# Performance work log

Measured on AMD Instinct MI355X. Metric: run time of the kernel, lower is better.

The kernel has to match this reference:

```python
import jax, jax.numpy as jnp
import numpy as np

B, T = 32, 64
I, O, H = 64, 64, 512
N, W = 128, 64           # memory slots, slot width
IF = 3 * W + 6           # interface size


def setup_inputs() -> dict:
    key = jax.random.key(0)
    ks = jax.random.split(key, 6)
    s = 0.05
    return {
        "x": jax.random.normal(ks[0], (B, T, I), jnp.float32),
        "W_ih": jax.random.normal(ks[1], (4 * H, I + W), jnp.float32) * s,
        "W_hh": jax.random.normal(ks[2], (4 * H, H), jnp.float32) * s,
        "b_ih": jnp.zeros((4 * H,), jnp.float32),
        "b_hh": jnp.zeros((4 * H,), jnp.float32),
        "W_if": jax.random.normal(ks[3], (IF, H), jnp.float32) * s,
        "b_if": jnp.zeros((IF,), jnp.float32),
        "W_out": jax.random.normal(ks[4], (O, H + W), jnp.float32) * s,
        "b_out": jnp.zeros((O,), jnp.float32),
    }


def reference(x, W_ih, W_hh, b_ih, b_hh, W_if, b_if, W_out, b_out):
    Bb, Tt, _ = x.shape
    dt = x.dtype
    eye = jnp.eye(N, dtype=dt)
    batch_idx = jnp.arange(Bb)[:, None]

    def step(carry, x_t):
        h, c, mem, usage, prec, link, rw, rvec = carry
        # --- LSTM controller (PyTorch gate order i,f,g,o) ---
        inp = jnp.concatenate([x_t, rvec], axis=-1)
        gates = inp @ W_ih.T + h @ W_hh.T + b_ih + b_hh
        i_g, f_g, g_g, o_g = jnp.split(gates, 4, axis=-1)
        c = jax.nn.sigmoid(f_g) * c + jax.nn.sigmoid(i_g) * jnp.tanh(g_g)
        h = jax.nn.sigmoid(o_g) * jnp.tanh(c)
        itf = h @ W_if.T + b_if
        # --- parse interface ---
        erase = jax.nn.sigmoid(itf[:, :W])
        wvec = itf[:, W:2 * W]
        wg = jax.nn.sigmoid(itf[:, 2 * W])
        ag = jax.nn.sigmoid(itf[:, 2 * W + 1])
        rstr = jnp.log1p(jnp.exp(itf[:, 3 * W + 2]))  # softplus
        # --- allocation weighting (sort usage asc, shifted cumprod, scatter) ---
        idx = jnp.argsort(usage, axis=-1)
        usage_sorted = jnp.take_along_axis(usage, idx, axis=-1)
        cprod = jnp.cumprod(usage_sorted, axis=-1)
        cprod = jnp.concatenate([jnp.ones((Bb, 1), dt), cprod[:, :-1]], axis=-1)
        alloc_in_order = (1.0 - usage_sorted) * cprod
        alloc = jnp.zeros_like(usage).at[batch_idx, idx].set(alloc_in_order)
        ww = wg[:, None] * ag[:, None] * alloc  # [B,N]
        # --- erase + add write ---
        mem = mem * (1.0 - ww[:, :, None] * erase[:, None, :]) + ww[:, :, None] * wvec[:, None, :]
        usage = usage + (1.0 - usage) * ww
        # --- temporal link / precedence ---
        ww_ij = ww[:, :, None] + ww[:, None, :]
        link = (1.0 - ww_ij) * link + prec[:, :, None] * ww[:, None, :]
        link = link * (1.0 - eye)
        prec = (1.0 - ww.sum(-1, keepdims=True)) * prec + ww
        # --- read weights (NOTE: source uses itf[:, :W] as read key) ---
        rmode = jax.nn.softmax(itf[:, -3:], axis=-1)
        rkey = itf[:, :W]
        dot = jnp.einsum('bw,bnw->bn', rkey, mem)
        kn = jnp.linalg.norm(rkey, axis=-1, keepdims=True) + 1e-8
        mn = jnp.linalg.norm(mem, axis=-1) + 1e-8
        cw = jax.nn.softmax(dot / (kn * mn) * rstr[:, None], axis=-1)
        bw = jnp.einsum('bnm,bn->bm', link, rw)   # link^T @ rw
        fw = jnp.einsum('bnm,bm->bn', link, rw)   # link @ rw
        wts = rmode[:, 0:1] * bw + rmode[:, 1:2] * fw + rmode[:, 2:3] * cw + 1e-8
        wts = wts / wts.sum(-1, keepdims=True)
        rvec = jnp.einsum('bn,bnw->bw', wts, mem)
        out = jnp.concatenate([h, rvec], axis=-1) @ W_out.T + b_out
        return (h, c, mem, usage, prec, link, wts, rvec), out

    z = lambda *s: jnp.zeros(s, dt)
    carry0 = (z(Bb, H), z(Bb, H), z(Bb, N, W), z(Bb, N), z(Bb, N), z(Bb, N, N), z(Bb, N), z(Bb, W))
    _, outs = jax.lax.scan(step, carry0, jnp.swapaxes(x, 0, 1))
    return jnp.swapaxes(outs, 0, 1)  # [B,T,O]
```

## Files before the change

### kernel.cpp

```cpp
#include <hip/hip_runtime.h>
#include <math.h>

#define Bb 32
#define Tt 64
#define Ii 64
#define Oo 64
#define Hh 512
#define Nn 128
#define Wd 64
#define IFs 198
#define KV 640
#define G4 2048

#define NP1 128
#define NWG 160
#define NT 512
#define VST2 648

#define P2_MEM    0
#define P2_H      8320
#define P2_SCR    8896
#define P2_ITF    10944
#define P2_ERASE  11168
#define P2_WVEC   11232
#define P2_USAGE  11296
#define P2_PREC   11424
#define P2_RW     11552
#define P2_WW     11680
#define P2_SCAN   11808
#define P2_SS     11936
#define P2_SCAL   12064
#define P2_BIF    12080
#define P2_ALLOC  12304
#define P1_WIF    0
#define P1_BS     13464
#define P1_V      13720
#define P1_CC     15016
#define P1_HSL    15144
#define P1_PACC   15272
#define SMEM_FLOATS 17352
#define SMEM_BYTES (SMEM_FLOATS * 4)

#define S_WWSUM 0

__device__ __align__(16) float g_WT[KV * G4];
__device__ __align__(16) float g_bsum[G4];
typedef unsigned long long u64;
__device__ u64 g_h64[2 * Bb * Hh];
__device__ u64 g_rv64[Bb * Wd];
__device__ u64 g_if64[Bb * 8 * 200];

__device__ __forceinline__ float sigf(float v) { return 1.f / (1.f + expf(-v)); }

__device__ __forceinline__ u64 ldrelax(const u64* p) {
  return __hip_atomic_load(p, __ATOMIC_RELAXED, __HIP_MEMORY_SCOPE_AGENT);
}
__device__ __forceinline__ void tstore(u64* p, unsigned tag, float v) {
  u64 val = ((u64)tag << 32) | (u64)__float_as_uint(v);
  __hip_atomic_store(p, val, __ATOMIC_RELAXED, __HIP_MEMORY_SCOPE_AGENT);
}
__device__ __forceinline__ float fixwait(const u64* p, u64 v, unsigned tag) {
  while ((unsigned)(v >> 32) != tag) {
    __builtin_amdgcn_s_sleep(1);
    v = ldrelax(p);
  }
  return __uint_as_float((unsigned)(v & 0xffffffffu));
}

#define TIN 512
__global__ __launch_bounds__(TIN) void dnc_init(const float* __restrict__ W_ih,
                                                const float* __restrict__ W_hh,
                                                const float* __restrict__ b_ih,
                                                const float* __restrict__ b_hh) {
  __shared__ float tile[64][65];
  const int tid = threadIdx.x;
  int i0 = blockIdx.x * blockDim.x + tid;
  int st = gridDim.x * blockDim.x;
  for (int idx = i0; idx < G4; idx += st) g_bsum[idx] = b_ih[idx] + b_hh[idx];
  for (int idx = i0; idx < 2 * Bb * Hh; idx += st) g_h64[idx] = 0ull;
  for (int idx = i0; idx < Bb * Wd; idx += st) g_rv64[idx] = 0ull;
  for (int idx = i0; idx < Bb * 8 * 200; idx += st) g_if64[idx] = 0ull;

  for (int tileId = blockIdx.x; tileId < 320; tileId += gridDim.x) {
    int tc = tileId >> 5, tj = tileId & 31;
    for (int k = tid; k < 64 * 64; k += TIN) {
      int r = k >> 6, cl = k & 63;
      int j = tj * 64 + r, c = tc * 64 + cl;
      tile[r][cl] = (c < 128) ? W_ih[j * 128 + c] : W_hh[j * 512 + (c - 128)];
    }
    __syncthreads();
    for (int k = tid; k < 64 * 64; k += TIN) {
      int cl = k >> 6, rjj = k & 63;
      int c = tc * 64 + cl;
      int rp;
      if (c < 64) rp = (c >> 4) * 160 + 128 + (c & 15);
      else if (c < 128) { int cc = c - 64; rp = (cc >> 4) * 160 + 144 + (cc & 15); }
      else { int u = c - 128; rp = (u >> 7) * 160 + (u & 127); }
      g_WT[(size_t)rp * G4 + tj * 64 + rjj] = tile[rjj][cl];
    }
    __syncthreads();
  }
}

__global__ __launch_bounds__(NT) void dnc_main(const float* __restrict__ x,
                                               const float* __restrict__ W_if,
                                               const float* __restrict__ b_if,
                                               const float* __restrict__ W_out,
                                               const float* __restrict__ b_out,
                                               float* __restrict__ out) {
  extern __shared__ float sm[];
  const int tid = threadIdx.x;
  const int wg = blockIdx.x;

  if (wg < NP1) {
    const int jb = wg & 7;
    const int bb = wg >> 3;
    const int b0 = bb * 2;
    for (int i = tid; i < IFs * 64; i += NT) {
      int o = i >> 6, c = i & 63;
      sm[P1_WIF + o * 68 + c] = W_if[(size_t)o * Hh + jb * 64 + c];
    }
    if (tid < 64) {
      int gq = tid >> 4, m = tid & 15;
      ((float4*)(sm + P1_BS))[tid] = ((const float4*)g_bsum)[gq * 128 + jb * 16 + m];
    }
    if (tid < 128) sm[P1_CC + tid] = 0.f;
    __syncthreads();

    for (int t = 0; t < Tt; ++t) {
      {
        const u64* hsrc = g_h64 + (size_t)((t + 1) & 1) * (Bb * Hh);
        const int u = tid;
        const u64* a0 = hsrc + (size_t)b0 * Hh + u;
        const u64* a1 = hsrc + (size_t)(b0 + 1) * Hh + u;
        u64 v0 = ldrelax(a0), v1 = ldrelax(a1);
        float h0 = fixwait(a0, v0, (unsigned)t);
        float h1 = fixwait(a1, v1, (unsigned)t);
        const int rp = (u >> 7) * 160 + (u & 127);
        sm[P1_V + rp] = h0;
        sm[P1_V + VST2 + rp] = h1;
        if (tid < 128) {
          const int bl2 = tid >> 6, i = tid & 63;
          float xv = x[((size_t)(b0 + bl2) * Tt + t) * Ii + i];
          sm[P1_V + bl2 * VST2 + (i >> 4) * 160 + 128 + (i & 15)] = xv;
        }
      }
      __syncthreads();

      {
        const int fc = tid & 63, bl = (tid >> 6) & 1, ks = tid >> 7;
        const int lane = tid & 63;
        const int fcol = (fc >> 4) * 128 + jb * 16 + (fc & 15);
        const float* va = sm + P1_V + bl * VST2 + ks * 160;
        const float4* wp = (const float4*)g_WT + (size_t)(ks * 160) * (G4 / 4) + fcol;
        float4 a = {0.f, 0.f, 0.f, 0.f};
#pragma unroll 8
        for (int r = 0; r < 144; ++r) {
          float4 w4 = wp[(size_t)r * (G4 / 4)];
          float fv = va[r];
          a.x += w4.x * fv; a.y += w4.y * fv; a.z += w4.z * fv; a.w += w4.w * fv;
        }
        if (lane < 16) {
          const u64* rp = g_rv64 + (size_t)(b0 + bl) * Wd + ks * 16 + lane;
          float rv = fixwait(rp, ldrelax(rp), (unsigned)t);
          sm[P1_V + bl * VST2 + ks * 160 + 144 + lane] = rv;
        }
#pragma unroll
        for (int r = 144; r < 160; ++r) {
          float4 w4 = wp[(size_t)r * (G4 / 4)];
          float fv = va[r];
          a.x += w4.x * fv; a.y += w4.y * fv; a.z += w4.z * fv; a.w += w4.w * fv;
        }
        ((float4*)(sm + P1_PACC))[(ks * 2 + bl) * 65 + fc] = a;
      }
      __syncthreads();
      if (tid < 128) {
        const int bl = tid >> 6, l = tid & 63;
        const float* pb = sm + P1_PACC + bl * 260 + l;
        float gv0 = 0.f, gv1 = 0.f, gv2 = 0.f, gv3 = 0.f;
#pragma unroll
        for (int ks = 0; ks < 4; ++ks) {
          const float* pk = pb + ks * 520;
          gv0 += pk[0];
          gv1 += pk[64];
          gv2 += pk[128];
          gv3 += pk[192];
        }
        float ig = gv0 + sm[P1_BS + l];
        float fg = gv1 + sm[P1_BS + 64 + l];
        float gg = gv2 + sm[P1_BS + 128 + l];
        float og = gv3 + sm[P1_BS + 192 + l];
        float co = sm[P1_CC + bl * 64 + l];
        float cn = sigf(fg) * co + sigf(ig) * tanhf(gg);
        float hn = sigf(og) * tanhf(cn);
        sm[P1_CC + bl * 64 + l] = cn;
        sm[P1_HSL + bl * 64 + l] = hn;
        tstore(g_h64 + (size_t)(t & 1) * (Bb * Hh) + (size_t)(b0 + bl) * Hh + jb * 64 + l,
               (unsigned)(t + 1), hn);
      }
      __syncthreads();
      if (tid < 2 * IFs) {
        const int o = tid >> 1, bl = tid & 1;
        const float4* wr = (const float4*)(sm + P1_WIF + o * 68);
        const float4* h4 = (const float4*)(sm + P1_HSL + bl * 64);
        float acc = 0.f;
#pragma unroll 8
        for (int c4 = 0; c4 < 16; ++c4) {
          float4 w = wr[c4]; float4 h = h4[c4];
          acc += w.x * h.x + w.y * h.y + w.z * h.z + w.w * h.w;
        }
        tstore(g_if64 + ((size_t)(b0 + bl) * 8 + jb) * 200 + o, (unsigned)(t + 1), acc);
      }
    }
  } else {
    const int b = wg - NP1;
    float* SCR = sm + P2_SCR;
    float regL[32], regLT[32];
#pragma unroll
    for (int k = 0; k < 32; ++k) { regL[k] = 0.f; regLT[k] = 0.f; }
    for (int i = tid; i < Nn * 65; i += NT) sm[P2_MEM + i] = 0.f;
    if (tid < 128) { sm[P2_USAGE + tid] = 0.f; sm[P2_PREC + tid] = 0.f; sm[P2_RW + tid] = 0.f; }
    if (tid < IFs) sm[P2_BIF + tid] = b_if[tid];
    __syncthreads();
    if (tid < 64) {
      const int li = tid, i0 = 2 * li, i1 = i0 + 1;
      float u0 = sm[P2_USAGE + i0], u1 = sm[P2_USAGE + i1];
      int r0 = 0, r1 = 0;
      for (int jc = 0; jc < 32; ++jc) {
        float4 uj4 = *(const float4*)(sm + P2_USAGE + jc * 4);
#pragma unroll
        for (int e = 0; e < 4; ++e) {
          float uj = (&uj4.x)[e];
          int j = jc * 4 + e;
          r0 += (uj < u0 || (uj == u0 && j < i0)) ? 1 : 0;
          r1 += (uj < u1 || (uj == u1 && j < i1)) ? 1 : 0;
        }
      }
      sm[P2_SS + r0] = u0;
      sm[P2_SS + r1] = u1;
      float s0 = sm[P2_SS + i0], s1 = sm[P2_SS + i1];
      float p = s0 * s1;
#pragma unroll
      for (int off = 1; off < 64; off <<= 1) {
        float v = __shfl_up(p, off, 64);
        if (li >= off) p *= v;
      }
      float E = __shfl_up(p, 1, 64);
      if (li == 0) E = 1.f;
      sm[P2_SCAN + i0] = E * s0;
      sm[P2_SCAN + i1] = E * s0 * s1;
      float ex0 = (r0 > 0) ? sm[P2_SCAN + r0 - 1] : 1.f;
      float ex1 = (r1 > 0) ? sm[P2_SCAN + r1 - 1] : 1.f;
      sm[P2_ALLOC + i0] = (1.f - u0) * ex0;
      sm[P2_ALLOC + i1] = (1.f - u1) * ex1;
    }
    __syncthreads();

    for (int t = 0; t < Tt; ++t) {
      if (tid < 2 * IFs) {
        const int o = tid >> 1, hf = tid & 1;
        const u64* src = g_if64 + ((size_t)b * 8 + hf * 4) * 200 + o;
        u64 a0 = ldrelax(src), a1 = ldrelax(src + 200),
            a2 = ldrelax(src + 400), a3 = ldrelax(src + 600);
        float s = fixwait(src, a0, (unsigned)(t + 1))
                + fixwait(src + 200, a1, (unsigned)(t + 1))
                + fixwait(src + 400, a2, (unsigned)(t + 1))
                + fixwait(src + 600, a3, (unsigned)(t + 1));
        s += __shfl_xor(s, 1, 64);
        if (hf == 0) sm[P2_ITF + o] = s + sm[P2_BIF + o];
      }
      __syncthreads();
      float kn_r = 0.f, rstr_r = 0.f, rm0_r = 0.f, rm1_r = 0.f, rm2_r = 0.f;
      if (tid < 64) {
        const int li = tid, i0 = 2 * li, i1 = i0 + 1;
        float wgag = sigf(sm[P2_ITF + 128]) * sigf(sm[P2_ITF + 129]);
        float rs = sm[P2_ITF + 194];
        rstr_r = (rs > 20.f) ? rs : log1pf(expf(rs));
        float m0 = sm[P2_ITF + 195], m1 = sm[P2_ITF + 196], m2 = sm[P2_ITF + 197];
        float mx = fmaxf(m0, fmaxf(m1, m2));
        float e0 = expf(m0 - mx), e1 = expf(m1 - mx), e2 = expf(m2 - mx);
        float es = e0 + e1 + e2;
        rm0_r = e0 / es; rm1_r = e1 / es; rm2_r = e2 / es;
        float rk = sm[P2_ITF + li];
        sm[P2_ERASE + li] = sigf(rk);
        sm[P2_WVEC + li] = sm[P2_ITF + 64 + li];
        float sq = rk * rk;
#pragma unroll
        for (int off = 32; off > 0; off >>= 1) sq += __shfl_xor(sq, off, 64);
        kn_r = sqrtf(sq) + 1e-8f;
        float u0 = sm[P2_USAGE + i0], u1 = sm[P2_USAGE + i1];
        float w0 = wgag * sm[P2_ALLOC + i0];
        float w1 = wgag * sm[P2_ALLOC + i1];
        sm[P2_WW + i0] = w0; sm[P2_WW + i1] = w1;
        sm[P2_USAGE + i0] = u0 + (1.f - u0) * w0;
        sm[P2_USAGE + i1] = u1 + (1.f - u1) * w1;
        float wws = w0 + w1;
#pragma unroll
        for (int off = 32; off > 0; off >>= 1) wws += __shfl_xor(wws, off, 64);
        if (li == 0) sm[P2_SCAL + S_WWSUM] = wws;
      }
      __syncthreads();
      {
        const int n = tid & 127, ws = tid >> 7;
        float4 er[4], wv[4], kf[4];
#pragma unroll
        for (int r = 0; r < 4; ++r) {
          er[r] = *(const float4*)(sm + P2_ERASE + ws * 16 + r * 4);
          wv[r] = *(const float4*)(sm + P2_WVEC + ws * 16 + r * 4);
          kf[r] = *(const float4*)(sm + P2_ITF + ws * 16 + r * 4);
        }
        float wwn = sm[P2_WW + n];
        float dotp = 0.f, mnp = 0.f;
        const int base = P2_MEM + n * 65 + ws * 16;
#pragma unroll
        for (int q = 0; q < 16; ++q) {
          float m = sm[base + q];
          float ee = (&er[q >> 2].x)[q & 3];
          float vv = (&wv[q >> 2].x)[q & 3];
          float kk = (&kf[q >> 2].x)[q & 3];
          m = m * (1.f - wwn * ee) + wwn * vv;
          sm[base + q] = m;
          dotp += kk * m;
          mnp += m * m;
        }
        SCR[ws * 128 + n] = dotp;
        SCR[512 + ws * 128 + n] = mnp;
        const int m = n, ns = ws;
        float wwm = wwn;
        float prn = sm[P2_PREC + m];
        float bwp = 0.f, fwp = 0.f;
#pragma unroll
        for (int kq = 0; kq < 8; ++kq) {
          float4 ww4 = *(const float4*)(sm + P2_WW + ns * 32 + kq * 4);
          float4 pr4 = *(const float4*)(sm + P2_PREC + ns * 32 + kq * 4);
          float4 rw4 = *(const float4*)(sm + P2_RW + ns * 32 + kq * 4);
#pragma unroll
          for (int e = 0; e < 4; ++e) {
            int k = kq * 4 + e;
            int nn = ns * 32 + k;
            float wwo = (&ww4.x)[e];
            float pro = (&pr4.x)[e];
            float rwo = (&rw4.x)[e];
            float L = regL[k];
            L = (1.f - wwo - wwm) * L + pro * wwm;
            if (nn == m) L = 0.f;
            regL[k] = L;
            bwp += L * rwo;
            float LT = regLT[k];
            LT = (1.f - wwm - wwo) * LT + prn * wwo;
            if (nn == m) LT = 0.f;
            regLT[k] = LT;
            fwp += LT * rwo;
          }
        }
        SCR[1024 + ns * 128 + m] = bwp;
        SCR[1536 + ns * 128 + m] = fwp;
      }
      __syncthreads();
      if (tid < 64) {
        int i0 = 2 * tid, i1 = i0 + 1;
        float d0 = SCR[i0] + SCR[128 + i0] + SCR[256 + i0] + SCR[384 + i0];
        float d1 = SCR[i1] + SCR[128 + i1] + SCR[256 + i1] + SCR[384 + i1];
        float mn0 = sqrtf(SCR[512 + i0] + SCR[640 + i0] + SCR[768 + i0] + SCR[896 + i0]) + 1e-8f;
        float mn1 = sqrtf(SCR[512 + i1] + SCR[640 + i1] + SCR[768 + i1] + SCR[896 + i1]) + 1e-8f;
        float bw0 = SCR[1024 + i0] + SCR[1152 + i0] + SCR[1280 + i0] + SCR[1408 + i0];
        float bw1 = SCR[1024 + i1] + SCR[1152 + i1] + SCR[1280 + i1] + SCR[1408 + i1];
        float fw0 = SCR[1536 + i0] + SCR[1664 + i0] + SCR[1792 + i0] + SCR[1920 + i0];
        float fw1 = SCR[1536 + i1] + SCR[1664 + i1] + SCR[1792 + i1] + SCR[1920 + i1];
        float q0 = d0 / (kn_r * mn0) * rstr_r;
        float q1 = d1 / (kn_r * mn1) * rstr_r;
        float mx = fmaxf(q0, q1);
#pragma unroll
        for (int off = 32; off > 0; off >>= 1) mx = fmaxf(mx, __shfl_xor(mx, off, 64));
        float e0 = expf(q0 - mx), e1 = expf(q1 - mx);
        float es = e0 + e1;
#pragma unroll
        for (int off = 32; off > 0; off >>= 1) es += __shfl_xor(es, off, 64);
        float wv0 = rm0_r * bw0 + rm1_r * fw0 + rm2_r * (e0 / es) + 1e-8f;
        float wv1 = rm0_r * bw1 + rm1_r * fw1 + rm2_r * (e1 / es) + 1e-8f;
        float wsum = wv0 + wv1;
#pragma unroll
        for (int off = 32; off > 0; off >>= 1) wsum += __shfl_xor(wsum, off, 64);
        sm[P2_RW + i0] = wv0 / wsum;
        sm[P2_RW + i1] = wv1 / wsum;
      }
      __syncthreads();
      {
        const int w = tid & 63, ns8 = tid >> 6;
        float4 rw4[4];
#pragma unroll
        for (int r = 0; r < 4; ++r)
          rw4[r] = *(const float4*)(sm + P2_RW + ns8 * 16 + r * 4);
        float p = 0.f;
#pragma unroll
        for (int k = 0; k < 16; ++k)
          p += (&rw4[k >> 2].x)[k & 3] * sm[P2_MEM + (ns8 * 16 + k) * 65 + w];
        SCR[ns8 * 64 + w] = p;
      }
      __syncthreads();
      if (tid < 64) {
        float r = 0.f;
#pragma unroll
        for (int s2 = 0; s2 < 8; ++s2) r += SCR[s2 * 64 + tid];
        sm[P2_H + 512 + tid] = r;
        tstore(g_rv64 + (size_t)b * Wd + tid, (unsigned)(t + 1), r);
      } else if (tid < 320) {
        const int idx = tid - 64;
        const u64* hsrc = g_h64 + (size_t)(t & 1) * (Bb * Hh) + (size_t)b * Hh;
        const u64* a0 = hsrc + idx * 2;
        const u64* a1 = hsrc + idx * 2 + 1;
        u64 v0 = ldrelax(a0), v1 = ldrelax(a1);
        sm[P2_H + idx * 2] = fixwait(a0, v0, (unsigned)(t + 1));
        sm[P2_H + idx * 2 + 1] = fixwait(a1, v1, (unsigned)(t + 1));
      } else if (tid < 384) {
        const int li = tid - 320, i0 = 2 * li, i1 = i0 + 1;
        float u0 = sm[P2_USAGE + i0], u1 = sm[P2_USAGE + i1];
        int r0 = 0, r1 = 0;
        for (int jc = 0; jc < 32; ++jc) {
          float4 uj4 = *(const float4*)(sm + P2_USAGE + jc * 4);
#pragma unroll
          for (int e = 0; e < 4; ++e) {
            float uj = (&uj4.x)[e];
            int j = jc * 4 + e;
            r0 += (uj < u0 || (uj == u0 && j < i0)) ? 1 : 0;
            r1 += (uj < u1 || (uj == u1 && j < i1)) ? 1 : 0;
          }
        }
        sm[P2_SS + r0] = u0;
        sm[P2_SS + r1] = u1;
        float s0 = sm[P2_SS + i0], s1 = sm[P2_SS + i1];
        float p = s0 * s1;
#pragma unroll
        for (int off = 1; off < 64; off <<= 1) {
          float v = __shfl_up(p, off, 64);
          if (li >= off) p *= v;
        }
        float E = __shfl_up(p, 1, 64);
        if (li == 0) E = 1.f;
        sm[P2_SCAN + i0] = E * s0;
        sm[P2_SCAN + i1] = E * s0 * s1;
        float ex0 = (r0 > 0) ? sm[P2_SCAN + r0 - 1] : 1.f;
        float ex1 = (r1 > 0) ? sm[P2_SCAN + r1 - 1] : 1.f;
        sm[P2_ALLOC + i0] = (1.f - u0) * ex0;
        sm[P2_ALLOC + i1] = (1.f - u1) * ex1;
      } else {
        const int n = tid - 384;
        float wws = sm[P2_SCAL + S_WWSUM];
        sm[P2_PREC + n] = (1.f - wws) * sm[P2_PREC + n] + sm[P2_WW + n];
      }
      __syncthreads();
      {
        const int o = tid >> 3, seg = tid & 7;
        const float4* wrow = (const float4*)(W_out + (size_t)o * 576) + seg * 18;
        const float4* hb = (const float4*)(sm + P2_H) + seg * 18;
        float p = 0.f;
#pragma unroll
        for (int q = 0; q < 18; ++q) {
          float4 w = wrow[q]; float4 h = hb[q];
          p += w.x * h.x + w.y * h.y + w.z * h.z + w.w * h.w;
        }
        p += __shfl_down(p, 4, 8);
        p += __shfl_down(p, 2, 8);
        p += __shfl_down(p, 1, 8);
        if (seg == 0) out[((size_t)b * Tt + t) * Oo + o] = p + b_out[o];
      }
    }
  }
}

extern "C" void kernel_launch(void* const* d_in, const int* in_sizes, int n_in,
                              void* d_out, int out_size, void* d_ws, size_t ws_size,
                              hipStream_t stream) {
  (void)in_sizes; (void)n_in; (void)d_ws; (void)ws_size; (void)out_size;
  const float* x    = (const float*)d_in[0];
  const float* W_ih = (const float*)d_in[1];
  const float* W_hh = (const float*)d_in[2];
  const float* b_ih = (const float*)d_in[3];
  const float* b_hh = (const float*)d_in[4];
  const float* W_if = (const float*)d_in[5];
  const float* b_if = (const float*)d_in[6];
  const float* W_out = (const float*)d_in[7];
  const float* b_out = (const float*)d_in[8];
  float* out = (float*)d_out;

  dnc_init<<<320, TIN, 0, stream>>>(W_ih, W_hh, b_ih, b_hh);

  hipFuncSetAttribute((const void*)dnc_main,
                      hipFuncAttributeMaxDynamicSharedMemorySize, SMEM_BYTES);

  void* args[] = {(void*)&x, (void*)&W_if, (void*)&b_if,
                  (void*)&W_out, (void*)&b_out, (void*)&out};
  hipLaunchCooperativeKernel((void*)dnc_main, dim3(NWG), dim3(NT), args,
                             SMEM_BYTES, stream);
}
```

Baseline: 881.4 us.

## Reorganize LSTM gate GEMV to share weight loads across both batch rows

Moves the input vector to an interleaved layout that pairs the two batch rows, and repacks W_T rows in plain order (h first, then x, then rvec). Each thread now handles both batch rows and two column groups, so every weight float4 it loads is reused twice. The K dimension is split 16 ways instead of 4, which gives shorter loops but a larger partial-sum reduction and more shared memory. The rvec wait moves to a single group of threads before the loop. The shared-memory footprint grows.

```diff
diff --git a/kernel.cpp b/kernel.cpp
--- a/kernel.cpp
+++ b/kernel.cpp
@@ -15,7 +15,6 @@
 #define NP1 128
 #define NWG 160
 #define NT 512
-#define VST2 648
 
 #define P2_MEM    0
 #define P2_H      8320
@@ -38,7 +37,7 @@
 #define P1_CC     15016
 #define P1_HSL    15144
 #define P1_PACC   15272
-#define SMEM_FLOATS 17352
+#define SMEM_FLOATS 23592
 #define SMEM_BYTES (SMEM_FLOATS * 4)
 
 #define S_WWSUM 0
@@ -92,10 +91,7 @@
     for (int k = tid; k < 64 * 64; k += TIN) {
       int cl = k >> 6, rjj = k & 63;
       int c = tc * 64 + cl;
-      int rp;
-      if (c < 64) rp = (c >> 4) * 160 + 128 + (c & 15);
-      else if (c < 128) { int cc = c - 64; rp = (cc >> 4) * 160 + 144 + (cc & 15); }
-      else { int u = c - 128; rp = (u >> 7) * 160 + (u & 127); }
+      int rp = (c < 128) ? (512 + c) : (c - 128);
       g_WT[(size_t)rp * G4 + tj * 64 + rjj] = tile[rjj][cl];
     }
     __syncthreads();
@@ -134,44 +130,50 @@
         const u64* a0 = hsrc + (size_t)b0 * Hh + u;
         const u64* a1 = hsrc + (size_t)(b0 + 1) * Hh + u;
         u64 v0 = ldrelax(a0), v1 = ldrelax(a1);
-        float h0 = fixwait(a0, v0, (unsigned)t);
-        float h1 = fixwait(a1, v1, (unsigned)t);
-        const int rp = (u >> 7) * 160 + (u & 127);
-        sm[P1_V + rp] = h0;
-        sm[P1_V + VST2 + rp] = h1;
+        float2 hh;
+        hh.x = fixwait(a0, v0, (unsigned)t);
+        hh.y = fixwait(a1, v1, (unsigned)t);
+        *(float2*)(sm + P1_V + u * 2) = hh;
         if (tid < 128) {
           const int bl2 = tid >> 6, i = tid & 63;
           float xv = x[((size_t)(b0 + bl2) * Tt + t) * Ii + i];
-          sm[P1_V + bl2 * VST2 + (i >> 4) * 160 + 128 + (i & 15)] = xv;
+          sm[P1_V + (512 + i) * 2 + bl2] = xv;
         }
       }
       __syncthreads();
 
       {
-        const int fc = tid & 63, bl = (tid >> 6) & 1, ks = tid >> 7;
-        const int lane = tid & 63;
-        const int fcol = (fc >> 4) * 128 + jb * 16 + (fc & 15);
-        const float* va = sm + P1_V + bl * VST2 + ks * 160;
-        const float4* wp = (const float4*)g_WT + (size_t)(ks * 160) * (G4 / 4) + fcol;
-        float4 a = {0.f, 0.f, 0.f, 0.f};
-#pragma unroll 8
-        for (int r = 0; r < 144; ++r) {
-          float4 w4 = wp[(size_t)r * (G4 / 4)];
-          float fv = va[r];
-          a.x += w4.x * fv; a.y += w4.y * fv; a.z += w4.z * fv; a.w += w4.w * fv;
-        }
-        if (lane < 16) {
-          const u64* rp = g_rv64 + (size_t)(b0 + bl) * Wd + ks * 16 + lane;
-          float rv = fixwait(rp, ldrelax(rp), (unsigned)t);
-          sm[P1_V + bl * VST2 + ks * 160 + 144 + lane] = rv;
-        }
-#pragma unroll
-        for (int r = 144; r < 160; ++r) {
-          float4 w4 = wp[(size_t)r * (G4 / 4)];
-          float fv = va[r];
-          a.x += w4.x * fv; a.y += w4.y * fv; a.z += w4.z * fv; a.w += w4.w * fv;
-        }
-        ((float4*)(sm + P1_PACC))[(ks * 2 + bl) * 65 + fc] = a;
+        const int fg = tid & 31, ks = tid >> 5;
+        const int fcolA = ((fg >> 4) * 128) + jb * 16 + (fg & 15);
+        const float* v2 = sm + P1_V + ks * 80;
+        const float4* wpA = (const float4*)g_WT + (size_t)(ks * 40) * 512 + fcolA;
+        if (ks >= 14) {
+          const int j = tid & 63;
+          const u64* r0 = g_rv64 + (size_t)b0 * Wd + j;
+          const u64* r1 = g_rv64 + (size_t)(b0 + 1) * Wd + j;
+          u64 u0 = ldrelax(r0), u1 = ldrelax(r1);
+          float2 rv;
+          rv.x = fixwait(r0, u0, (unsigned)t);
+          rv.y = fixwait(r1, u1, (unsigned)t);
+          *(float2*)(sm + P1_V + (576 + j) * 2) = rv;
+        }
+        float4 aA0 = {0.f, 0.f, 0.f, 0.f}, aA1 = {0.f, 0.f, 0.f, 0.f};
+        float4 aB0 = {0.f, 0.f, 0.f, 0.f}, aB1 = {0.f, 0.f, 0.f, 0.f};
+#pragma unroll 4
+        for (int r = 0; r < 40; ++r) {
+          float4 wA = wpA[(size_t)r * 512];
+          float4 wB = wpA[(size_t)r * 512 + 256];
+          float2 vv = *(const float2*)(v2 + r * 2);
+          aA0.x += wA.x * vv.x; aA0.y += wA.y * vv.x; aA0.z += wA.z * vv.x; aA0.w += wA.w * vv.x;
+          aA1.x += wA.x * vv.y; aA1.y += wA.y * vv.y; aA1.z += wA.z * vv.y; aA1.w += wA.w * vv.y;
+          aB0.x += wB.x * vv.x; aB0.y += wB.y * vv.x; aB0.z += wB.z * vv.x; aB0.w += wB.w * vv.x;
+          aB1.x += wB.x * vv.y; aB1.y += wB.y * vv.y; aB1.z += wB.z * vv.y; aB1.w += wB.w * vv.y;
+        }
+        float4* pacc = (float4*)(sm + P1_PACC);
+        pacc[(ks * 2 + 0) * 65 + fg] = aA0;
+        pacc[(ks * 2 + 1) * 65 + fg] = aA1;
+        pacc[(ks * 2 + 0) * 65 + fg + 32] = aB0;
+        pacc[(ks * 2 + 1) * 65 + fg + 32] = aB1;
       }
       __syncthreads();
       if (tid < 128) {
@@ -179,7 +181,7 @@
         const float* pb = sm + P1_PACC + bl * 260 + l;
         float gv0 = 0.f, gv1 = 0.f, gv2 = 0.f, gv3 = 0.f;
 #pragma unroll
-        for (int ks = 0; ks < 4; ++ks) {
+        for (int ks = 0; ks < 16; ++ks) {
           const float* pk = pb + ks * 520;
           gv0 += pk[0];
           gv1 += pk[64];
```

Measured after the change: 873.5 us. No clear change (-0.9%).
